# Optimization experiments

Hardware: AMD Instinct MI355X
Metric: run time of the kernel (lower is better)

## Reference

```python
import jax, jax.numpy as jnp
import numpy as np

HEADS = 8
GS = 128  # group_size


def _windows(x, ng, gs):
    # x: [B, (ng+1)*gs, ...] -> overlapping windows [B, ng, 2*gs, ...]
    B = x.shape[0]
    r = x.reshape((B, ng + 1, gs) + x.shape[2:])
    return jnp.concatenate([r[:, :ng], r[:, 1:ng + 1]], axis=2)


def iasa_forward(normed_x, idx_last, k_global, v_global, sorted_belong_idx,
                 prev_attn_map, Wq, Wk, Wv, Wproj):
    B, N, dim = normed_x.shape
    h = HEADS
    gs = min(N, GS)
    ng = (N + gs - 1) // gs
    pad_n = ng * gs - N

    q = normed_x @ Wq  # [B,N,qk_dim]
    k = normed_x @ Wk
    v = normed_x @ Wv
    q = jnp.take_along_axis(q, idx_last, axis=1)
    k = jnp.take_along_axis(k, idx_last, axis=1)
    v = jnp.take_along_axis(v, idx_last, axis=1)

    dq = q.shape[-1] // h
    dv = v.shape[-1] // h

    # query groups: pad with flipped tail, [B, ng, h, gs, dq]
    pq = jnp.concatenate([q, q[:, N - pad_n:N][:, ::-1]], axis=1)
    pq = pq.reshape(B, ng, gs, h, dq).transpose(0, 1, 3, 2, 4)

    # key/value overlapping windows of size 2*gs, stride gs
    pk = jnp.concatenate([k, k[:, N - pad_n - gs:N][:, ::-1]], axis=1)  # [B,(ng+1)*gs,qk]
    pk = _windows(pk, ng, gs).reshape(B, ng, 2 * gs, h, dq).transpose(0, 1, 3, 2, 4)
    pv = jnp.concatenate([v, v[:, N - pad_n - gs:N][:, ::-1]], axis=1)
    pv = _windows(pv, ng, gs).reshape(B, ng, 2 * gs, h, dv).transpose(0, 1, 3, 2, 4)

    # belong-group mask
    iq = jnp.concatenate([sorted_belong_idx, sorted_belong_idx[:, N - pad_n:N][:, ::-1]], axis=1)
    iq = iq.reshape(B, ng, gs)
    ik = jnp.concatenate([sorted_belong_idx, sorted_belong_idx[:, N - pad_n - gs:N][:, ::-1]], axis=1)
    ik = _windows(ik, ng, gs)  # [B, ng, 2*gs]
    mask = (iq[:, :, :, None] == ik[:, :, None, :])[:, :, None]  # [B,ng,1,gs,2gs]

    scale = dq ** (-0.5)
    logits = jnp.einsum('bnhqd,bnhkd->bnhqk', pq, pk) * scale
    logits = jnp.where(mask, logits, -jnp.inf)
    probs = jax.nn.softmax(logits, axis=-1)

    alpha = 0.5
    fused = alpha * prev_attn_map + (1.0 - alpha) * probs
    fused = jnp.where(mask, fused, 0.0)
    fused = fused / (jnp.sum(fused, axis=-1, keepdims=True) + 1e-9)

    out1 = jnp.einsum('bnhqk,bnhkd->bnhqd', fused, pv)

    # global attention term (standard SDPA against shared global tokens)
    s2 = jnp.einsum('bnhqd,hmd->bnhqm', pq, k_global) * scale
    p2 = jax.nn.softmax(s2, axis=-1)
    out2 = jnp.einsum('bnhqm,hmd->bnhqd', p2, v_global)

    out = out1 + out2  # [B,ng,h,gs,dv]
    out = out.transpose(0, 1, 3, 2, 4).reshape(B, ng * gs, h * dv)[:, :N]

    # scatter back: result[b, idx_last[b,n], :] = out[b, n, :] (base = out itself)
    b_idx = jnp.arange(B)[:, None]
    out = out.at[b_idx, idx_last[:, :, 0], :].set(out)
    out = out @ Wproj
    return out, fused


def setup_inputs() -> dict:
    key = jax.random.key(0)
    ks = jax.random.split(key, 10)
    B, N, dim, qk_dim, h, M = 2, 16384, 256, 256, HEADS, 64
    ng, gs = N // GS, GS
    normed_x = jax.random.normal(ks[0], (B, N, dim), dtype=jnp.float32)
    # permutation indices (typical: sort order), shape [B,N,1]
    perm = jax.vmap(lambda k: jax.random.permutation(k, N))(jax.random.split(ks[1], B))
    idx_last = perm[:, :, None].astype(jnp.int64)
    k_global = jax.random.normal(ks[2], (h, M, qk_dim // h), dtype=jnp.float32)
    v_global = jax.random.normal(ks[3], (h, M, dim // h), dtype=jnp.float32)
    sorted_belong_idx = jnp.sort(jax.random.randint(ks[4], (B, N), 0, 128), axis=-1).astype(jnp.int64)
    prev_attn_map = jax.random.uniform(ks[5], (B, ng, h, gs, 2 * gs), dtype=jnp.float32)
    Wq = jax.random.normal(ks[6], (dim, qk_dim), dtype=jnp.float32) * (dim ** -0.5)
    Wk = jax.random.normal(ks[7], (dim, qk_dim), dtype=jnp.float32) * (dim ** -0.5)
    Wv = jax.random.normal(ks[8], (dim, dim), dtype=jnp.float32) * (dim ** -0.5)
    Wproj = jax.random.normal(ks[9], (dim, dim), dtype=jnp.float32) * (dim ** -0.5)
    return {"normed_x": normed_x, "idx_last": idx_last, "k_global": k_global,
            "v_global": v_global, "sorted_belong_idx": sorted_belong_idx,
            "prev_attn_map": prev_attn_map, "Wq": Wq, "Wk": Wk, "Wv": Wv, "Wproj": Wproj}


def reference(normed_x, idx_last, k_global, v_global, sorted_belong_idx,
              prev_attn_map, Wq, Wk, Wv, Wproj):
    return iasa_forward(normed_x, idx_last, k_global, v_global,
                        sorted_belong_idx, prev_attn_map, Wq, Wk, Wv, Wproj)
```

## Files before the change

### kernel.cpp

```cpp
#include <hip/hip_runtime.h>

typedef __attribute__((ext_vector_type(8))) short bf16x8;
typedef __attribute__((ext_vector_type(8))) unsigned short u16x8;
typedef __attribute__((ext_vector_type(4))) float f32x4;

#define B_ 2
#define N_ 16384
#define DIM_ 256
#define H_ 8
#define DH_ 32
#define GS_ 128
#define NG_ 128
#define M_ 64
#define SCALE 0.17677669529663687f

#define KW 40
#define FW 328
#define XW 264

__device__ __forceinline__ unsigned short f2bf(float x) {
  union { float f; unsigned u; } v; v.f = x;
  unsigned r = v.u + 0x7fffu + ((v.u >> 16) & 1u);
  return (unsigned short)(r >> 16);
}

__global__ void k0_transpose(const float* __restrict__ W0, const float* __restrict__ W1,
                             const float* __restrict__ W2, const float* __restrict__ W3,
                             unsigned short* __restrict__ WT) {
  __shared__ float t[32][33];
  const float* W = (blockIdx.z == 0) ? W0 : (blockIdx.z == 1) ? W1 : (blockIdx.z == 2) ? W2 : W3;
  unsigned short* D = WT + (size_t)blockIdx.z * 65536;
  int tx = threadIdx.x & 31, ty = threadIdx.x >> 5;
  int r0 = blockIdx.y * 32, c0 = blockIdx.x * 32;
#pragma unroll
  for (int k = 0; k < 4; ++k)
    t[ty + 8 * k][tx] = W[(size_t)(r0 + ty + 8 * k) * 256 + c0 + tx];
  __syncthreads();
#pragma unroll
  for (int k = 0; k < 4; ++k)
    D[(size_t)(c0 + ty + 8 * k) * 256 + r0 + tx] = f2bf(t[tx][ty + 8 * k]);
}

__global__ void k0_kgvg(const float* __restrict__ kgf, const float* __restrict__ vgf,
                        unsigned short* __restrict__ kgb, unsigned short* __restrict__ vgt) {
  int i = blockIdx.x * 256 + threadIdx.x;
  if (i < H_ * M_ * DH_) {
    kgb[i] = f2bf(kgf[i]);
    int hh = i >> 11, rem = i & 2047, d = rem >> 6, mm = rem & 63;
    vgt[i] = f2bf(vgf[((size_t)hh * M_ + mm) * DH_ + d]);
  }
}

__global__ __launch_bounds__(512) void k1_qkv(const float* __restrict__ x, const int* __restrict__ idx,
                                              const unsigned short* __restrict__ WT,
                                              unsigned short* __restrict__ qg,
                                              unsigned short* __restrict__ kg,
                                              unsigned short* __restrict__ vg) {
  __shared__ __attribute__((aligned(16))) unsigned short Xs[128 * XW];
  const int tid = threadIdx.x;
  const int brow0 = blockIdx.x * 128;
  const int b = brow0 >> 14;
  {
    int r = tid >> 2, part = tid & 3;
    int src = idx[brow0 + r];
    const float* xp = x + ((size_t)b * N_ + src) * DIM_ + part * 64;
    unsigned short* dp = &Xs[r * XW + part * 64];
#pragma unroll
    for (int i = 0; i < 8; ++i) {
      float4 v0 = ((const float4*)xp)[2 * i];
      float4 v1 = ((const float4*)xp)[2 * i + 1];
      u16x8 o;
      o[0] = f2bf(v0.x); o[1] = f2bf(v0.y); o[2] = f2bf(v0.z); o[3] = f2bf(v0.w);
      o[4] = f2bf(v1.x); o[5] = f2bf(v1.y); o[6] = f2bf(v1.z); o[7] = f2bf(v1.w);
      *(u16x8*)(dp + i * 8) = o;
    }
  }
  __syncthreads();
  const int lane = tid & 63, wid = tid >> 6;
  const int l15 = lane & 15, l4 = lane >> 4;
  const int qr0 = wid * 16;
  bf16x8 a[8];
#pragma unroll
  for (int ks = 0; ks < 8; ++ks)
    a[ks] = *(const bf16x8*)&Xs[(qr0 + l15) * XW + ks * 32 + l4 * 8];
#pragma unroll
  for (int w = 0; w < 3; ++w) {
    const unsigned short* WTm = WT + w * 65536;
    unsigned short* dst = (w == 0) ? qg : (w == 1) ? kg : vg;
    for (int ct = 0; ct < 16; ++ct) {
      f32x4 acc = {0.f, 0.f, 0.f, 0.f};
#pragma unroll
      for (int ks = 0; ks < 8; ++ks) {
        bf16x8 bfr = *(const bf16x8*)&WTm[(ct * 16 + l15) * 256 + ks * 32 + l4 * 8];
        acc = __builtin_amdgcn_mfma_f32_16x16x32_bf16(a[ks], bfr, acc, 0, 0, 0);
      }
      int col = ct * 16 + l15, hh = col >> 5, cc = col & 31;
#pragma unroll
      for (int r = 0; r < 4; ++r) {
        int grow = brow0 + qr0 + l4 * 4 + r;
        int n = grow & (N_ - 1);
        dst[(((size_t)((grow >> 14) * H_ + hh)) * N_ + n) * DH_ + cc] = f2bf(acc[r]);
      }
    }
  }
}

__global__ __launch_bounds__(512) void k2_attn(
    const unsigned short* __restrict__ qg, const unsigned short* __restrict__ kgv,
    const unsigned short* __restrict__ vgv, const unsigned short* __restrict__ kglob,
    const unsigned short* __restrict__ vgt, const int* __restrict__ sbi,
    const float* __restrict__ prev, float* __restrict__ fusedOut,
    unsigned short* __restrict__ outPre) {
  __shared__ __attribute__((aligned(16))) unsigned short Qs[128 * KW];
  __shared__ __attribute__((aligned(16))) unsigned short Ks[256 * KW];
  __shared__ __attribute__((aligned(16))) unsigned short Vts[32 * FW];
  __shared__ __attribute__((aligned(16))) unsigned short Kgs[64 * KW];
  __shared__ int bq[128];
  __shared__ int bk[256];
  __shared__ __attribute__((aligned(16))) unsigned short Fs[128 * FW];

  const int tid = threadIdx.x;
  const int h = blockIdx.x & 7;
  const int g = (blockIdx.x >> 3) & 127;
  const int b = blockIdx.x >> 10;
  const int n0 = g * GS_;
  const size_t headBase = ((size_t)b * H_ + h) * (size_t)N_ * DH_;

  {
    int r = tid >> 2, q = tid & 3;
    *(u16x8*)&Qs[r * KW + q * 8] = *(const u16x8*)&qg[headBase + (size_t)(n0 + r) * DH_ + q * 8];
  }
#pragma unroll
  for (int it = 0; it < 2; ++it) {
    int slot = tid + it * 512;
    int w = slot >> 2, q = slot & 3;
    int srcn = (w < 128 || g < NG_ - 1) ? (n0 + w) : (N_ - 1 - (w - 128));
    *(u16x8*)&Ks[w * KW + q * 8] = *(const u16x8*)&kgv[headBase + (size_t)srcn * DH_ + q * 8];
  }
  {
    int w = tid >> 1, hh = tid & 1;
    int srcn = (w < 128 || g < NG_ - 1) ? (n0 + w) : (N_ - 1 - (w - 128));
    const unsigned short* src = &vgv[headBase + (size_t)srcn * DH_ + hh * 16];
    u16x8 v0 = *(const u16x8*)src;
    u16x8 v1 = *(const u16x8*)(src + 8);
#pragma unroll
    for (int j = 0; j < 8; ++j) {
      Vts[(hh * 16 + j) * FW + w] = v0[j];
      Vts[(hh * 16 + 8 + j) * FW + w] = v1[j];
    }
  }
  if (tid < 128) {
    int d = tid >> 2, q = tid & 3;
    const unsigned short* src = &vgt[((size_t)h * DH_ + d) * M_ + q * 16];
    *(u16x8*)&Vts[d * FW + 256 + q * 16] = *(const u16x8*)src;
    *(u16x8*)&Vts[d * FW + 256 + q * 16 + 8] = *(const u16x8*)(src + 8);
  }
  if (tid < 256) {
    int m = tid >> 2, q = tid & 3;
    *(u16x8*)&Kgs[m * KW + q * 8] = *(const u16x8*)&kglob[((size_t)h * M_ + m) * DH_ + q * 8];
  }
  if (tid < 128) bq[tid] = sbi[b * N_ + n0 + tid];
  if (tid >= 256) {
    int w = tid - 256;
    int srcn = (w < 128 || g < NG_ - 1) ? (n0 + w) : (N_ - 1 - (w - 128));
    bk[w] = sbi[b * N_ + srcn];
  }
  __syncthreads();

  const int lane = tid & 63, wid = tid >> 6;
  const int l15 = lane & 15, l4 = lane >> 4;
  const int qr0 = wid * 16;

  bf16x8 qa = *(const bf16x8*)&Qs[(qr0 + l15) * KW + l4 * 8];

  f32x4 c[16];
#pragma unroll
  for (int ct = 0; ct < 16; ++ct) {
    bf16x8 kb = *(const bf16x8*)&Ks[(ct * 16 + l15) * KW + l4 * 8];
    f32x4 z = {0.f, 0.f, 0.f, 0.f};
    c[ct] = __builtin_amdgcn_mfma_f32_16x16x32_bf16(qa, kb, z, 0, 0, 0);
  }

  int bkv[16];
#pragma unroll
  for (int ct = 0; ct < 16; ++ct) bkv[ct] = bk[ct * 16 + l15];
  int myq[4];
#pragma unroll
  for (int r = 0; r < 4; ++r) myq[r] = bq[qr0 + l4 * 4 + r];

  float mx[4] = {-1e30f, -1e30f, -1e30f, -1e30f};
#pragma unroll
  for (int ct = 0; ct < 16; ++ct)
#pragma unroll
    for (int r = 0; r < 4; ++r) {
      float v = c[ct][r] * SCALE;
      c[ct][r] = v;
      if (bkv[ct] == myq[r]) mx[r] = fmaxf(mx[r], v);
    }
#pragma unroll
  for (int r = 0; r < 4; ++r) {
    mx[r] = fmaxf(mx[r], __shfl_xor(mx[r], 1));
    mx[r] = fmaxf(mx[r], __shfl_xor(mx[r], 2));
    mx[r] = fmaxf(mx[r], __shfl_xor(mx[r], 4));
    mx[r] = fmaxf(mx[r], __shfl_xor(mx[r], 8));
  }
  float sm[4] = {0.f, 0.f, 0.f, 0.f};
#pragma unroll
  for (int ct = 0; ct < 16; ++ct)
#pragma unroll
    for (int r = 0; r < 4; ++r) {
      float p = (bkv[ct] == myq[r]) ? __expf(c[ct][r] - mx[r]) : 0.f;
      c[ct][r] = p;
      sm[r] += p;
    }
#pragma unroll
  for (int r = 0; r < 4; ++r) {
    sm[r] += __shfl_xor(sm[r], 1);
    sm[r] += __shfl_xor(sm[r], 2);
    sm[r] += __shfl_xor(sm[r], 4);
    sm[r] += __shfl_xor(sm[r], 8);
  }
  float inv[4];
#pragma unroll
  for (int r = 0; r < 4; ++r) inv[r] = 1.f / sm[r];

  const size_t pbase = ((((size_t)b * NG_ + g) * H_ + h) * GS_) * (size_t)(2 * GS_);
  float fs[4] = {0.f, 0.f, 0.f, 0.f};
#pragma unroll
  for (int ct = 0; ct < 16; ++ct)
#pragma unroll
    for (int r = 0; r < 4; ++r) {
      int row = qr0 + l4 * 4 + r;
      float pr = prev[pbase + (size_t)row * 256 + ct * 16 + l15];
      float f = (bkv[ct] == myq[r]) ? (0.5f * pr + 0.5f * c[ct][r] * inv[r]) : 0.f;
      c[ct][r] = f;
      fs[r] += f;
    }
#pragma unroll
  for (int r = 0; r < 4; ++r) {
    fs[r] += __shfl_xor(fs[r], 1);
    fs[r] += __shfl_xor(fs[r], 2);
    fs[r] += __shfl_xor(fs[r], 4);
    fs[r] += __shfl_xor(fs[r], 8);
  }
  float fn[4];
#pragma unroll
  for (int r = 0; r < 4; ++r) fn[r] = 1.f / (fs[r] + 1e-9f);
#pragma unroll
  for (int ct = 0; ct < 16; ++ct)
#pragma unroll
    for (int r = 0; r < 4; ++r) {
      int row = qr0 + l4 * 4 + r;
      float f = c[ct][r] * fn[r];
      fusedOut[pbase + (size_t)row * 256 + ct * 16 + l15] = f;
      Fs[row * FW + ct * 16 + l15] = f2bf(f);
    }

  f32x4 c2[4];
#pragma unroll
  for (int ct = 0; ct < 4; ++ct) {
    bf16x8 kb = *(const bf16x8*)&Kgs[(ct * 16 + l15) * KW + l4 * 8];
    f32x4 z = {0.f, 0.f, 0.f, 0.f};
    c2[ct] = __builtin_amdgcn_mfma_f32_16x16x32_bf16(qa, kb, z, 0, 0, 0);
  }
  float m2[4] = {-1e30f, -1e30f, -1e30f, -1e30f};
#pragma unroll
  for (int ct = 0; ct < 4; ++ct)
#pragma unroll
    for (int r = 0; r < 4; ++r) {
      float v = c2[ct][r] * SCALE;
      c2[ct][r] = v;
      m2[r] = fmaxf(m2[r], v);
    }
#pragma unroll
  for (int r = 0; r < 4; ++r) {
    m2[r] = fmaxf(m2[r], __shfl_xor(m2[r], 1));
    m2[r] = fmaxf(m2[r], __shfl_xor(m2[r], 2));
    m2[r] = fmaxf(m2[r], __shfl_xor(m2[r], 4));
    m2[r] = fmaxf(m2[r], __shfl_xor(m2[r], 8));
  }
  float s2[4] = {0.f, 0.f, 0.f, 0.f};
#pragma unroll
  for (int ct = 0; ct < 4; ++ct)
#pragma unroll
    for (int r = 0; r < 4; ++r) {
      float p = __expf(c2[ct][r] - m2[r]);
      c2[ct][r] = p;
      s2[r] += p;
    }
#pragma unroll
  for (int r = 0; r < 4; ++r) {
    s2[r] += __shfl_xor(s2[r], 1);
    s2[r] += __shfl_xor(s2[r], 2);
    s2[r] += __shfl_xor(s2[r], 4);
    s2[r] += __shfl_xor(s2[r], 8);
  }
#pragma unroll
  for (int ct = 0; ct < 4; ++ct)
#pragma unroll
    for (int r = 0; r < 4; ++r) {
      int row = qr0 + l4 * 4 + r;
      Fs[row * FW + 256 + ct * 16 + l15] = f2bf(c2[ct][r] / s2[r]);
    }

  __syncthreads();

  f32x4 acc0 = {0.f, 0.f, 0.f, 0.f}, acc1 = {0.f, 0.f, 0.f, 0.f};
#pragma unroll
  for (int kt = 0; kt < 10; ++kt) {
    bf16x8 af = *(const bf16x8*)&Fs[(qr0 + l15) * FW + kt * 32 + l4 * 8];
    bf16x8 b0 = *(const bf16x8*)&Vts[l15 * FW + kt * 32 + l4 * 8];
    bf16x8 b1 = *(const bf16x8*)&Vts[(16 + l15) * FW + kt * 32 + l4 * 8];
    acc0 = __builtin_amdgcn_mfma_f32_16x16x32_bf16(af, b0, acc0, 0, 0, 0);
    acc1 = __builtin_amdgcn_mfma_f32_16x16x32_bf16(af, b1, acc1, 0, 0, 0);
  }
#pragma unroll
  for (int r = 0; r < 4; ++r) {
    int row = qr0 + l4 * 4 + r;
    size_t orow = ((size_t)b * N_ + n0 + row) * DIM_ + h * DH_;
    outPre[orow + l15] = f2bf(acc0[r]);
    outPre[orow + 16 + l15] = f2bf(acc1[r]);
  }
}

__global__ __launch_bounds__(512) void k3_proj(const unsigned short* __restrict__ outPre,
                                               const unsigned short* __restrict__ WpT,
                                               const int* __restrict__ idx,
                                               float* __restrict__ out) {
  __shared__ __attribute__((aligned(16))) unsigned short As[128 * XW];
  const int tid = threadIdx.x;
  const int brow0 = blockIdx.x * 128;
  {
    int r = tid >> 2, part = tid & 3;
    const unsigned short* sp = &outPre[(size_t)(brow0 + r) * 256 + part * 64];
    unsigned short* dp = &As[r * XW + part * 64];
#pragma unroll
    for (int i = 0; i < 8; ++i)
      *(u16x8*)(dp + i * 8) = *(const u16x8*)(sp + i * 8);
  }
  __syncthreads();
  const int lane = tid & 63, wid = tid >> 6;
  const int l15 = lane & 15, l4 = lane >> 4;
  const int qr0 = wid * 16;
  bf16x8 a[8];
#pragma unroll
  for (int ks = 0; ks < 8; ++ks)
    a[ks] = *(const bf16x8*)&As[(qr0 + l15) * XW + ks * 32 + l4 * 8];
  int destRow[4];
#pragma unroll
  for (int r = 0; r < 4; ++r) destRow[r] = idx[brow0 + qr0 + l4 * 4 + r];
  const int b = brow0 >> 14;
  for (int ct = 0; ct < 16; ++ct) {
    f32x4 acc = {0.f, 0.f, 0.f, 0.f};
#pragma unroll
    for (int ks = 0; ks < 8; ++ks) {
      bf16x8 bfr = *(const bf16x8*)&WpT[(ct * 16 + l15) * 256 + ks * 32 + l4 * 8];
      acc = __builtin_amdgcn_mfma_f32_16x16x32_bf16(a[ks], bfr, acc, 0, 0, 0);
    }
#pragma unroll
    for (int r = 0; r < 4; ++r)
      out[((size_t)b * N_ + destRow[r]) * DIM_ + ct * 16 + l15] = acc[r];
  }
}

extern "C" void kernel_launch(void* const* d_in, const int* in_sizes, int n_in,
                              void* d_out, int out_size, void* d_ws, size_t ws_size,
                              hipStream_t stream) {
  const float* x    = (const float*)d_in[0];
  const int*   idx  = (const int*)d_in[1];
  const float* kgf  = (const float*)d_in[2];
  const float* vgf  = (const float*)d_in[3];
  const int*   sbi  = (const int*)d_in[4];
  const float* prev = (const float*)d_in[5];
  const float* Wq   = (const float*)d_in[6];
  const float* Wk   = (const float*)d_in[7];
  const float* Wv   = (const float*)d_in[8];
  const float* Wp   = (const float*)d_in[9];
  float* out = (float*)d_out;
  float* fusedOut = out + (size_t)B_ * N_ * DIM_;

  char* ws = (char*)d_ws;
  unsigned short* WT     = (unsigned short*)ws;
  unsigned short* kgb    = (unsigned short*)(ws + 524288);
  unsigned short* vgt    = (unsigned short*)(ws + 557056);
  unsigned short* qg     = (unsigned short*)(ws + 589824);
  unsigned short* kga    = qg  + (size_t)B_ * H_ * N_ * DH_;
  unsigned short* vga    = kga + (size_t)B_ * H_ * N_ * DH_;
  unsigned short* outPre = vga + (size_t)B_ * H_ * N_ * DH_;

  k0_transpose<<<dim3(8, 8, 4), 256, 0, stream>>>(Wq, Wk, Wv, Wp, WT);
  k0_kgvg<<<64, 256, 0, stream>>>(kgf, vgf, kgb, vgt);
  k1_qkv<<<256, 512, 0, stream>>>(x, idx, WT, qg, kga, vga);
  k2_attn<<<2048, 512, 0, stream>>>(qg, kga, vga, kgb, vgt, sbi, prev, fusedOut, outPre);
  k3_proj<<<256, 512, 0, stream>>>(outPre, WT + 3 * 65536, idx, out);
}
```

Before: 805.7 us.

## Rework attention kernel to register-resident transposed scores and transposed V layout

The attention kernel computes transposed score tiles (K×Q) so each lane owns one query row. Row sums come from two shuffles, and probabilities stay in registers packed as bf16. They are exchanged via ds_bpermute into MFMA A-operands, which drops the shared-memory staging of Q/K/V/F and the block barrier. The QKV projection now writes V pre-transposed (d-major) for direct vector loads, fuses the three weight GEMMs per column tile, and uses 64-row blocks of 256 threads, as does the output projection, which computes two column tiles per pass. The max-subtraction in softmax is removed, which risks overflow with large logits, and the fused map is rounded through bf16 before the fp32 output.

```diff
diff --git a/kernel.cpp b/kernel.cpp
--- a/kernel.cpp
+++ b/kernel.cpp
@@ -2,6 +2,7 @@
 
 typedef __attribute__((ext_vector_type(8))) short bf16x8;
 typedef __attribute__((ext_vector_type(8))) unsigned short u16x8;
+typedef __attribute__((ext_vector_type(4))) unsigned short u16x4;
 typedef __attribute__((ext_vector_type(4))) float f32x4;
 
 #define B_ 2
@@ -14,14 +15,36 @@
 #define M_ 64
 #define SCALE 0.17677669529663687f
 
-#define KW 40
-#define FW 328
 #define XW 264
 
 __device__ __forceinline__ unsigned short f2bf(float x) {
   union { float f; unsigned u; } v; v.f = x;
   unsigned r = v.u + 0x7fffu + ((v.u >> 16) & 1u);
   return (unsigned short)(r >> 16);
+}
+__device__ __forceinline__ float bf2f(unsigned us16) {
+  union { unsigned u; float f; } v; v.u = us16 << 16; return v.f;
+}
+__device__ __forceinline__ unsigned pack2(float a, float b) {
+  return (unsigned)f2bf(a) | ((unsigned)f2bf(b) << 16);
+}
+
+__device__ __forceinline__ bf16x8 xchg(unsigned loA, unsigned hiA, unsigned loB, unsigned hiB,
+                                       int idxA, int idxB, bool hiSel) {
+  unsigned a0 = (unsigned)__builtin_amdgcn_ds_bpermute(idxA, (int)loA);
+  unsigned a1 = (unsigned)__builtin_amdgcn_ds_bpermute(idxA, (int)loB);
+  unsigned b0 = (unsigned)__builtin_amdgcn_ds_bpermute(idxA, (int)hiA);
+  unsigned b1 = (unsigned)__builtin_amdgcn_ds_bpermute(idxA, (int)hiB);
+  unsigned c0 = (unsigned)__builtin_amdgcn_ds_bpermute(idxB, (int)loA);
+  unsigned c1 = (unsigned)__builtin_amdgcn_ds_bpermute(idxB, (int)loB);
+  unsigned d0 = (unsigned)__builtin_amdgcn_ds_bpermute(idxB, (int)hiA);
+  unsigned d1 = (unsigned)__builtin_amdgcn_ds_bpermute(idxB, (int)hiB);
+  union { unsigned u[4]; bf16x8 v; } U;
+  U.u[0] = hiSel ? a1 : a0;
+  U.u[1] = hiSel ? b1 : b0;
+  U.u[2] = hiSel ? c1 : c0;
+  U.u[3] = hiSel ? d1 : d0;
+  return U.v;
 }
 
 __global__ void k0_transpose(const float* __restrict__ W0, const float* __restrict__ W1,
@@ -51,14 +74,14 @@
   }
 }
 
-__global__ __launch_bounds__(512) void k1_qkv(const float* __restrict__ x, const int* __restrict__ idx,
+__global__ __launch_bounds__(256) void k1_qkv(const float* __restrict__ x, const int* __restrict__ idx,
                                               const unsigned short* __restrict__ WT,
                                               unsigned short* __restrict__ qg,
                                               unsigned short* __restrict__ kg,
-                                              unsigned short* __restrict__ vg) {
-  __shared__ __attribute__((aligned(16))) unsigned short Xs[128 * XW];
+                                              unsigned short* __restrict__ vgt2) {
+  __shared__ __attribute__((aligned(16))) unsigned short Xs[64 * XW];
   const int tid = threadIdx.x;
-  const int brow0 = blockIdx.x * 128;
+  const int brow0 = blockIdx.x * 64;
   const int b = brow0 >> 14;
   {
     int r = tid >> 2, part = tid & 3;
@@ -83,41 +106,40 @@
 #pragma unroll
   for (int ks = 0; ks < 8; ++ks)
     a[ks] = *(const bf16x8*)&Xs[(qr0 + l15) * XW + ks * 32 + l4 * 8];
-#pragma unroll
-  for (int w = 0; w < 3; ++w) {
-    const unsigned short* WTm = WT + w * 65536;
-    unsigned short* dst = (w == 0) ? qg : (w == 1) ? kg : vg;
-    for (int ct = 0; ct < 16; ++ct) {
-      f32x4 acc = {0.f, 0.f, 0.f, 0.f};
-#pragma unroll
-      for (int ks = 0; ks < 8; ++ks) {
-        bf16x8 bfr = *(const bf16x8*)&WTm[(ct * 16 + l15) * 256 + ks * 32 + l4 * 8];
-        acc = __builtin_amdgcn_mfma_f32_16x16x32_bf16(a[ks], bfr, acc, 0, 0, 0);
-      }
-      int col = ct * 16 + l15, hh = col >> 5, cc = col & 31;
-#pragma unroll
-      for (int r = 0; r < 4; ++r) {
-        int grow = brow0 + qr0 + l4 * 4 + r;
-        int n = grow & (N_ - 1);
-        dst[(((size_t)((grow >> 14) * H_ + hh)) * N_ + n) * DH_ + cc] = f2bf(acc[r]);
-      }
-    }
+  const int nbase = (brow0 + qr0 + l4 * 4) & (N_ - 1);
+  for (int ct = 0; ct < 16; ++ct) {
+    f32x4 accq = {0.f, 0.f, 0.f, 0.f};
+    f32x4 acck = {0.f, 0.f, 0.f, 0.f};
+    f32x4 accv = {0.f, 0.f, 0.f, 0.f};
+#pragma unroll
+    for (int ks = 0; ks < 8; ++ks) {
+      const unsigned short* wrow = &WT[(ct * 16 + l15) * 256 + ks * 32 + l4 * 8];
+      accq = __builtin_amdgcn_mfma_f32_16x16x32_bf16(a[ks], *(const bf16x8*)wrow, accq, 0, 0, 0);
+      acck = __builtin_amdgcn_mfma_f32_16x16x32_bf16(a[ks], *(const bf16x8*)(wrow + 65536), acck, 0, 0, 0);
+      accv = __builtin_amdgcn_mfma_f32_16x16x32_bf16(a[ks], *(const bf16x8*)(wrow + 131072), accv, 0, 0, 0);
+    }
+    int col = ct * 16 + l15, hh = col >> 5, cc = col & 31;
+    size_t qkbase = ((size_t)(b * H_ + hh)) * N_ * DH_ + cc;
+#pragma unroll
+    for (int r = 0; r < 4; ++r) {
+      size_t o = qkbase + (size_t)(nbase + r) * DH_;
+      qg[o] = f2bf(accq[r]);
+      kg[o] = f2bf(acck[r]);
+    }
+    u16x4 vv;
+    vv[0] = f2bf(accv[0]); vv[1] = f2bf(accv[1]); vv[2] = f2bf(accv[2]); vv[3] = f2bf(accv[3]);
+    *(u16x4*)&vgt2[((size_t)(b * H_ + hh) * DH_ + cc) * N_ + nbase] = vv;
   }
 }
 
 __global__ __launch_bounds__(512) void k2_attn(
-    const unsigned short* __restrict__ qg, const unsigned short* __restrict__ kgv,
-    const unsigned short* __restrict__ vgv, const unsigned short* __restrict__ kglob,
+    const unsigned short* __restrict__ qg, const unsigned short* __restrict__ kga,
+    const unsigned short* __restrict__ vgt2, const unsigned short* __restrict__ kglob,
     const unsigned short* __restrict__ vgt, const int* __restrict__ sbi,
     const float* __restrict__ prev, float* __restrict__ fusedOut,
     unsigned short* __restrict__ outPre) {
-  __shared__ __attribute__((aligned(16))) unsigned short Qs[128 * KW];
-  __shared__ __attribute__((aligned(16))) unsigned short Ks[256 * KW];
-  __shared__ __attribute__((aligned(16))) unsigned short Vts[32 * FW];
-  __shared__ __attribute__((aligned(16))) unsigned short Kgs[64 * KW];
-  __shared__ int bq[128];
-  __shared__ int bk[256];
-  __shared__ __attribute__((aligned(16))) unsigned short Fs[128 * FW];
+  __shared__ __attribute__((aligned(16))) int bq[128];
+  __shared__ __attribute__((aligned(16))) int bk[256];
 
   const int tid = threadIdx.x;
   const int h = blockIdx.x & 7;
@@ -126,42 +148,9 @@
   const int n0 = g * GS_;
   const size_t headBase = ((size_t)b * H_ + h) * (size_t)N_ * DH_;
 
-  {
-    int r = tid >> 2, q = tid & 3;
-    *(u16x8*)&Qs[r * KW + q * 8] = *(const u16x8*)&qg[headBase + (size_t)(n0 + r) * DH_ + q * 8];
-  }
-#pragma unroll
-  for (int it = 0; it < 2; ++it) {
-    int slot = tid + it * 512;
-    int w = slot >> 2, q = slot & 3;
-    int srcn = (w < 128 || g < NG_ - 1) ? (n0 + w) : (N_ - 1 - (w - 128));
-    *(u16x8*)&Ks[w * KW + q * 8] = *(const u16x8*)&kgv[headBase + (size_t)srcn * DH_ + q * 8];
-  }
-  {
-    int w = tid >> 1, hh = tid & 1;
-    int srcn = (w < 128 || g < NG_ - 1) ? (n0 + w) : (N_ - 1 - (w - 128));
-    const unsigned short* src = &vgv[headBase + (size_t)srcn * DH_ + hh * 16];
-    u16x8 v0 = *(const u16x8*)src;
-    u16x8 v1 = *(const u16x8*)(src + 8);
-#pragma unroll
-    for (int j = 0; j < 8; ++j) {
-      Vts[(hh * 16 + j) * FW + w] = v0[j];
-      Vts[(hh * 16 + 8 + j) * FW + w] = v1[j];
-    }
-  }
-  if (tid < 128) {
-    int d = tid >> 2, q = tid & 3;
-    const unsigned short* src = &vgt[((size_t)h * DH_ + d) * M_ + q * 16];
-    *(u16x8*)&Vts[d * FW + 256 + q * 16] = *(const u16x8*)src;
-    *(u16x8*)&Vts[d * FW + 256 + q * 16 + 8] = *(const u16x8*)(src + 8);
-  }
-  if (tid < 256) {
-    int m = tid >> 2, q = tid & 3;
-    *(u16x8*)&Kgs[m * KW + q * 8] = *(const u16x8*)&kglob[((size_t)h * M_ + m) * DH_ + q * 8];
-  }
   if (tid < 128) bq[tid] = sbi[b * N_ + n0 + tid];
-  if (tid >= 256) {
-    int w = tid - 256;
+  else if (tid < 384) {
+    int w = tid - 128;
     int srcn = (w < 128 || g < NG_ - 1) ? (n0 + w) : (N_ - 1 - (w - 128));
     bk[w] = sbi[b * N_ + srcn];
   }
@@ -170,166 +159,142 @@
   const int lane = tid & 63, wid = tid >> 6;
   const int l15 = lane & 15, l4 = lane >> 4;
   const int qr0 = wid * 16;
-
-  bf16x8 qa = *(const bf16x8*)&Qs[(qr0 + l15) * KW + l4 * 8];
-
-  f32x4 c[16];
-#pragma unroll
-  for (int ct = 0; ct < 16; ++ct) {
-    bf16x8 kb = *(const bf16x8*)&Ks[(ct * 16 + l15) * KW + l4 * 8];
+  const int q = qr0 + l15;
+
+  const bf16x8 qb = *(const bf16x8*)&qg[headBase + (size_t)(n0 + q) * DH_ + l4 * 8];
+  const int myb = bq[q];
+
+  unsigned pkl[16], pkh[16];
+  unsigned long long mbits = 0ull;
+  float sm = 0.f;
+#pragma unroll
+  for (int wt = 0; wt < 16; ++wt) {
+    int w = wt * 16 + l15;
+    int srcn = (w < 128 || g < NG_ - 1) ? (n0 + w) : (N_ - 1 - (w - 128));
+    bf16x8 ka = *(const bf16x8*)&kga[headBase + (size_t)srcn * DH_ + l4 * 8];
     f32x4 z = {0.f, 0.f, 0.f, 0.f};
-    c[ct] = __builtin_amdgcn_mfma_f32_16x16x32_bf16(qa, kb, z, 0, 0, 0);
-  }
-
-  int bkv[16];
-#pragma unroll
-  for (int ct = 0; ct < 16; ++ct) bkv[ct] = bk[ct * 16 + l15];
-  int myq[4];
-#pragma unroll
-  for (int r = 0; r < 4; ++r) myq[r] = bq[qr0 + l4 * 4 + r];
-
-  float mx[4] = {-1e30f, -1e30f, -1e30f, -1e30f};
-#pragma unroll
-  for (int ct = 0; ct < 16; ++ct)
-#pragma unroll
-    for (int r = 0; r < 4; ++r) {
-      float v = c[ct][r] * SCALE;
-      c[ct][r] = v;
-      if (bkv[ct] == myq[r]) mx[r] = fmaxf(mx[r], v);
-    }
+    f32x4 s = __builtin_amdgcn_mfma_f32_16x16x32_bf16(ka, qb, z, 0, 0, 0);
+    int4 kb = *(const int4*)&bk[wt * 16 + l4 * 4];
+    const int kbv[4] = {kb.x, kb.y, kb.z, kb.w};
+    float p[4];
+#pragma unroll
+    for (int r = 0; r < 4; ++r) {
+      bool m = (kbv[r] == myb);
+      p[r] = m ? __expf(s[r] * SCALE) : 0.f;
+      sm += p[r];
+      mbits |= (unsigned long long)(m ? 1 : 0) << (wt * 4 + r);
+    }
+    pkl[wt] = pack2(p[0], p[1]);
+    pkh[wt] = pack2(p[2], p[3]);
+  }
+
+  unsigned p2l[4], p2h[4];
+  float s2 = 0.f;
+#pragma unroll
+  for (int wt = 0; wt < 4; ++wt) {
+    bf16x8 ga = *(const bf16x8*)&kglob[((size_t)h * M_ + wt * 16 + l15) * DH_ + l4 * 8];
+    f32x4 z = {0.f, 0.f, 0.f, 0.f};
+    f32x4 s = __builtin_amdgcn_mfma_f32_16x16x32_bf16(ga, qb, z, 0, 0, 0);
+    float p[4];
+#pragma unroll
+    for (int r = 0; r < 4; ++r) {
+      p[r] = __expf(s[r] * SCALE);
+      s2 += p[r];
+    }
+    p2l[wt] = pack2(p[0], p[1]);
+    p2h[wt] = pack2(p[2], p[3]);
+  }
+
+  sm += __shfl_xor(sm, 16); sm += __shfl_xor(sm, 32);
+  s2 += __shfl_xor(s2, 16); s2 += __shfl_xor(s2, 32);
+  const float halfinv = 0.5f / sm;
+  const float invs2 = 1.f / s2;
+
+  const size_t pbase = (((size_t)(b * NG_ + g) * H_ + h) * GS_ + q) * (size_t)(2 * GS_) + l4 * 4;
+  float fs = 0.f;
+#pragma unroll
+  for (int wt = 0; wt < 16; ++wt) {
+    float4 pr = *(const float4*)&prev[pbase + wt * 16];
+    const float prv[4] = {pr.x, pr.y, pr.z, pr.w};
+    float p[4] = {bf2f(pkl[wt] & 0xffffu), bf2f(pkl[wt] >> 16),
+                  bf2f(pkh[wt] & 0xffffu), bf2f(pkh[wt] >> 16)};
+    float f[4];
+#pragma unroll
+    for (int r = 0; r < 4; ++r) {
+      bool m = (mbits >> (wt * 4 + r)) & 1ull;
+      f[r] = m ? (0.5f * prv[r] + halfinv * p[r]) : 0.f;
+      fs += f[r];
+    }
+    pkl[wt] = pack2(f[0], f[1]);
+    pkh[wt] = pack2(f[2], f[3]);
+  }
+  fs += __shfl_xor(fs, 16); fs += __shfl_xor(fs, 32);
+  const float fn = 1.f / (fs + 1e-9f);
+
+#pragma unroll
+  for (int wt = 0; wt < 16; ++wt) {
+    float4 o;
+    o.x = bf2f(pkl[wt] & 0xffffu) * fn;
+    o.y = bf2f(pkl[wt] >> 16) * fn;
+    o.z = bf2f(pkh[wt] & 0xffffu) * fn;
+    o.w = bf2f(pkh[wt] >> 16) * fn;
+    *(float4*)&fusedOut[pbase + wt * 16] = o;
+  }
+
+  const int idxA = (l15 + (l4 & 1) * 32) * 4;
+  const int idxB = idxA + 64;
+  const bool hiSel = (l4 >= 2);
+  f32x4 aw0 = {0.f, 0.f, 0.f, 0.f}, aw1 = {0.f, 0.f, 0.f, 0.f};
+  f32x4 ag0 = {0.f, 0.f, 0.f, 0.f}, ag1 = {0.f, 0.f, 0.f, 0.f};
+  const size_t vrow0 = ((size_t)(b * H_ + h) * DH_ + l15) * (size_t)N_;
+  const size_t vrow1 = vrow0 + (size_t)16 * N_;
+#pragma unroll
+  for (int kt = 0; kt < 8; ++kt) {
+    bf16x8 af = xchg(pkl[2 * kt], pkh[2 * kt], pkl[2 * kt + 1], pkh[2 * kt + 1], idxA, idxB, hiSel);
+    bf16x8 bv0, bv1;
+    if (g == NG_ - 1 && kt >= 4) {
+#pragma unroll
+      for (int j = 0; j < 8; ++j) {
+        int kp = kt * 32 + l4 * 8 + j;
+        int sn = N_ - 1 - (kp - 128);
+        bv0[j] = (short)vgt2[vrow0 + sn];
+        bv1[j] = (short)vgt2[vrow1 + sn];
+      }
+    } else {
+      bv0 = *(const bf16x8*)&vgt2[vrow0 + n0 + kt * 32 + l4 * 8];
+      bv1 = *(const bf16x8*)&vgt2[vrow1 + n0 + kt * 32 + l4 * 8];
+    }
+    aw0 = __builtin_amdgcn_mfma_f32_16x16x32_bf16(af, bv0, aw0, 0, 0, 0);
+    aw1 = __builtin_amdgcn_mfma_f32_16x16x32_bf16(af, bv1, aw1, 0, 0, 0);
+  }
+#pragma unroll
+  for (int kt = 0; kt < 2; ++kt) {
+    bf16x8 af = xchg(p2l[2 * kt], p2h[2 * kt], p2l[2 * kt + 1], p2h[2 * kt + 1], idxA, idxB, hiSel);
+    bf16x8 b0 = *(const bf16x8*)&vgt[((size_t)h * DH_ + l15) * M_ + kt * 32 + l4 * 8];
+    bf16x8 b1 = *(const bf16x8*)&vgt[((size_t)h * DH_ + 16 + l15) * M_ + kt * 32 + l4 * 8];
+    ag0 = __builtin_amdgcn_mfma_f32_16x16x32_bf16(af, b0, ag0, 0, 0, 0);
+    ag1 = __builtin_amdgcn_mfma_f32_16x16x32_bf16(af, b1, ag1, 0, 0, 0);
+  }
+
 #pragma unroll
   for (int r = 0; r < 4; ++r) {
-    mx[r] = fmaxf(mx[r], __shfl_xor(mx[r], 1));
-    mx[r] = fmaxf(mx[r], __shfl_xor(mx[r], 2));
-    mx[r] = fmaxf(mx[r], __shfl_xor(mx[r], 4));
-    mx[r] = fmaxf(mx[r], __shfl_xor(mx[r], 8));
-  }
-  float sm[4] = {0.f, 0.f, 0.f, 0.f};
-#pragma unroll
-  for (int ct = 0; ct < 16; ++ct)
-#pragma unroll
-    for (int r = 0; r < 4; ++r) {
-      float p = (bkv[ct] == myq[r]) ? __expf(c[ct][r] - mx[r]) : 0.f;
-      c[ct][r] = p;
-      sm[r] += p;
-    }
-#pragma unroll
-  for (int r = 0; r < 4; ++r) {
-    sm[r] += __shfl_xor(sm[r], 1);
-    sm[r] += __shfl_xor(sm[r], 2);
-    sm[r] += __shfl_xor(sm[r], 4);
-    sm[r] += __shfl_xor(sm[r], 8);
-  }
-  float inv[4];
-#pragma unroll
-  for (int r = 0; r < 4; ++r) inv[r] = 1.f / sm[r];
-
-  const size_t pbase = ((((size_t)b * NG_ + g) * H_ + h) * GS_) * (size_t)(2 * GS_);
-  float fs[4] = {0.f, 0.f, 0.f, 0.f};
-#pragma unroll
-  for (int ct = 0; ct < 16; ++ct)
-#pragma unroll
-    for (int r = 0; r < 4; ++r) {
-      int row = qr0 + l4 * 4 + r;
-      float pr = prev[pbase + (size_t)row * 256 + ct * 16 + l15];
-      float f = (bkv[ct] == myq[r]) ? (0.5f * pr + 0.5f * c[ct][r] * inv[r]) : 0.f;
-      c[ct][r] = f;
-      fs[r] += f;
-    }
-#pragma unroll
-  for (int r = 0; r < 4; ++r) {
-    fs[r] += __shfl_xor(fs[r], 1);
-    fs[r] += __shfl_xor(fs[r], 2);
-    fs[r] += __shfl_xor(fs[r], 4);
-    fs[r] += __shfl_xor(fs[r], 8);
-  }
-  float fn[4];
-#pragma unroll
-  for (int r = 0; r < 4; ++r) fn[r] = 1.f / (fs[r] + 1e-9f);
-#pragma unroll
-  for (int ct = 0; ct < 16; ++ct)
-#pragma unroll
-    for (int r = 0; r < 4; ++r) {
-      int row = qr0 + l4 * 4 + r;
-      float f = c[ct][r] * fn[r];
-      fusedOut[pbase + (size_t)row * 256 + ct * 16 + l15] = f;
-      Fs[row * FW + ct * 16 + l15] = f2bf(f);
-    }
-
-  f32x4 c2[4];
-#pragma unroll
-  for (int ct = 0; ct < 4; ++ct) {
-    bf16x8 kb = *(const bf16x8*)&Kgs[(ct * 16 + l15) * KW + l4 * 8];
-    f32x4 z = {0.f, 0.f, 0.f, 0.f};
-    c2[ct] = __builtin_amdgcn_mfma_f32_16x16x32_bf16(qa, kb, z, 0, 0, 0);
-  }
-  float m2[4] = {-1e30f, -1e30f, -1e30f, -1e30f};
-#pragma unroll
-  for (int ct = 0; ct < 4; ++ct)
-#pragma unroll
-    for (int r = 0; r < 4; ++r) {
-      float v = c2[ct][r] * SCALE;
-      c2[ct][r] = v;
-      m2[r] = fmaxf(m2[r], v);
-    }
-#pragma unroll
-  for (int r = 0; r < 4; ++r) {
-    m2[r] = fmaxf(m2[r], __shfl_xor(m2[r], 1));
-    m2[r] = fmaxf(m2[r], __shfl_xor(m2[r], 2));
-    m2[r] = fmaxf(m2[r], __shfl_xor(m2[r], 4));
-    m2[r] = fmaxf(m2[r], __shfl_xor(m2[r], 8));
-  }
-  float s2[4] = {0.f, 0.f, 0.f, 0.f};
-#pragma unroll
-  for (int ct = 0; ct < 4; ++ct)
-#pragma unroll
-    for (int r = 0; r < 4; ++r) {
-      float p = __expf(c2[ct][r] - m2[r]);
-      c2[ct][r] = p;
-      s2[r] += p;
-    }
-#pragma unroll
-  for (int r = 0; r < 4; ++r) {
-    s2[r] += __shfl_xor(s2[r], 1);
-    s2[r] += __shfl_xor(s2[r], 2);
-    s2[r] += __shfl_xor(s2[r], 4);
-    s2[r] += __shfl_xor(s2[r], 8);
-  }
-#pragma unroll
-  for (int ct = 0; ct < 4; ++ct)
-#pragma unroll
-    for (int r = 0; r < 4; ++r) {
-      int row = qr0 + l4 * 4 + r;
-      Fs[row * FW + 256 + ct * 16 + l15] = f2bf(c2[ct][r] / s2[r]);
-    }
-
-  __syncthreads();
-
-  f32x4 acc0 = {0.f, 0.f, 0.f, 0.f}, acc1 = {0.f, 0.f, 0.f, 0.f};
-#pragma unroll
-  for (int kt = 0; kt < 10; ++kt) {
-    bf16x8 af = *(const bf16x8*)&Fs[(qr0 + l15) * FW + kt * 32 + l4 * 8];
-    bf16x8 b0 = *(const bf16x8*)&Vts[l15 * FW + kt * 32 + l4 * 8];
-    bf16x8 b1 = *(const bf16x8*)&Vts[(16 + l15) * FW + kt * 32 + l4 * 8];
-    acc0 = __builtin_amdgcn_mfma_f32_16x16x32_bf16(af, b0, acc0, 0, 0, 0);
-    acc1 = __builtin_amdgcn_mfma_f32_16x16x32_bf16(af, b1, acc1, 0, 0, 0);
-  }
-#pragma unroll
-  for (int r = 0; r < 4; ++r) {
-    int row = qr0 + l4 * 4 + r;
-    size_t orow = ((size_t)b * N_ + n0 + row) * DIM_ + h * DH_;
-    outPre[orow + l15] = f2bf(acc0[r]);
-    outPre[orow + 16 + l15] = f2bf(acc1[r]);
-  }
-}
-
-__global__ __launch_bounds__(512) void k3_proj(const unsigned short* __restrict__ outPre,
+    float fnC = __shfl(fn, l4 * 4 + r);
+    float iC = __shfl(invs2, l4 * 4 + r);
+    int n = n0 + qr0 + l4 * 4 + r;
+    size_t o = ((size_t)b * N_ + n) * DIM_ + h * DH_ + l15;
+    outPre[o] = f2bf(fnC * aw0[r] + iC * ag0[r]);
+    outPre[o + 16] = f2bf(fnC * aw1[r] + iC * ag1[r]);
+  }
+}
+
+__global__ __launch_bounds__(256) void k3_proj(const unsigned short* __restrict__ outPre,
                                                const unsigned short* __restrict__ WpT,
                                                const int* __restrict__ idx,
                                                float* __restrict__ out) {
-  __shared__ __attribute__((aligned(16))) unsigned short As[128 * XW];
+  __shared__ __attribute__((aligned(16))) unsigned short As[64 * XW];
   const int tid = threadIdx.x;
-  const int brow0 = blockIdx.x * 128;
+  const int brow0 = blockIdx.x * 64;
+  const int b = brow0 >> 14;
   {
     int r = tid >> 2, part = tid & 3;
     const unsigned short* sp = &outPre[(size_t)(brow0 + r) * 256 + part * 64];
@@ -349,17 +314,21 @@
   int destRow[4];
 #pragma unroll
   for (int r = 0; r < 4; ++r) destRow[r] = idx[brow0 + qr0 + l4 * 4 + r];
-  const int b = brow0 >> 14;
-  for (int ct = 0; ct < 16; ++ct) {
-    f32x4 acc = {0.f, 0.f, 0.f, 0.f};
+  for (int ct2 = 0; ct2 < 8; ++ct2) {
+    f32x4 acc0 = {0.f, 0.f, 0.f, 0.f};
+    f32x4 acc1 = {0.f, 0.f, 0.f, 0.f};
 #pragma unroll
     for (int ks = 0; ks < 8; ++ks) {
-      bf16x8 bfr = *(const bf16x8*)&WpT[(ct * 16 + l15) * 256 + ks * 32 + l4 * 8];
-      acc = __builtin_amdgcn_mfma_f32_16x16x32_bf16(a[ks], bfr, acc, 0, 0, 0);
-    }
-#pragma unroll
-    for (int r = 0; r < 4; ++r)
-      out[((size_t)b * N_ + destRow[r]) * DIM_ + ct * 16 + l15] = acc[r];
+      const unsigned short* wrow = &WpT[(ct2 * 32 + l15) * 256 + ks * 32 + l4 * 8];
+      acc0 = __builtin_amdgcn_mfma_f32_16x16x32_bf16(a[ks], *(const bf16x8*)wrow, acc0, 0, 0, 0);
+      acc1 = __builtin_amdgcn_mfma_f32_16x16x32_bf16(a[ks], *(const bf16x8*)(wrow + 16 * 256), acc1, 0, 0, 0);
+    }
+#pragma unroll
+    for (int r = 0; r < 4; ++r) {
+      size_t o = ((size_t)b * N_ + destRow[r]) * DIM_ + ct2 * 32 + l15;
+      out[o] = acc0[r];
+      out[o + 16] = acc1[r];
+    }
   }
 }
 
@@ -385,12 +354,12 @@
   unsigned short* vgt    = (unsigned short*)(ws + 557056);
   unsigned short* qg     = (unsigned short*)(ws + 589824);
   unsigned short* kga    = qg  + (size_t)B_ * H_ * N_ * DH_;
-  unsigned short* vga    = kga + (size_t)B_ * H_ * N_ * DH_;
-  unsigned short* outPre = vga + (size_t)B_ * H_ * N_ * DH_;
+  unsigned short* vgt2   = kga + (size_t)B_ * H_ * N_ * DH_;
+  unsigned short* outPre = vgt2 + (size_t)B_ * H_ * N_ * DH_;
 
   k0_transpose<<<dim3(8, 8, 4), 256, 0, stream>>>(Wq, Wk, Wv, Wp, WT);
   k0_kgvg<<<64, 256, 0, stream>>>(kgf, vgf, kgb, vgt);
-  k1_qkv<<<256, 512, 0, stream>>>(x, idx, WT, qg, kga, vga);
-  k2_attn<<<2048, 512, 0, stream>>>(qg, kga, vga, kgb, vgt, sbi, prev, fusedOut, outPre);
-  k3_proj<<<256, 512, 0, stream>>>(outPre, WT + 3 * 65536, idx, out);
-}
+  k1_qkv<<<512, 256, 0, stream>>>(x, idx, WT, qg, kga, vgt2);
+  k2_attn<<<2048, 512, 0, stream>>>(qg, kga, vgt2, kgb, vgt, sbi, prev, fusedOut, outPre);
+  k3_proj<<<512, 256, 0, stream>>>(outPre, WT + 3 * 65536, idx, out);
+}
```

Measured after the change: 692.6 us. 1.16x faster.
